# Performance work log

Measured on AMD Instinct MI355X. Metric: run time of the kernel, lower is better.

Reference implementation:

```python
import jax, jax.numpy as jnp
import numpy as np


def _lstm_layer(xs, W_ih, W_hh, b):
    # xs: [T, B, D]; W_ih: [4H, D]; W_hh: [4H, H]; b: [4H] (b_ih + b_hh)
    T, B, _ = xs.shape
    H = W_hh.shape[1]
    # precompute input projection for all timesteps: [T, B, 4H]
    x_proj = jnp.einsum('tbd,gd->tbg', xs, W_ih) + b

    def step(carry, xp):
        h, c = carry
        gates = xp + h @ W_hh.T                      # [B, 4H]
        i, f, g, o = jnp.split(gates, 4, axis=-1)    # torch gate order i,f,g,o
        i = jax.nn.sigmoid(i)
        f = jax.nn.sigmoid(f)
        g = jnp.tanh(g)
        o = jax.nn.sigmoid(o)
        c = f * c + i * g
        h = o * jnp.tanh(c)
        return (h, c), h

    h0 = jnp.zeros((B, H), xs.dtype)
    c0 = jnp.zeros((B, H), xs.dtype)
    (h_T, c_T), outs = jax.lax.scan(step, (h0, c0), x_proj)
    return outs, h_T, c_T  # outs: [T, B, H]


def setup_inputs() -> dict:
    key = jax.random.key(0)
    ks = jax.random.split(key, 8)
    B, T, D, H, C = 64, 256, 512, 1024, 1000
    s = 0.05
    return {
        'x': jax.random.normal(ks[0], (B, T, D), jnp.float32),
        'W_ih0': jax.random.normal(ks[1], (4 * H, D), jnp.float32) * s,
        'W_hh0': jax.random.normal(ks[2], (4 * H, H), jnp.float32) * s,
        'b_ih0': jnp.zeros((4 * H,), jnp.float32),
        'b_hh0': jnp.zeros((4 * H,), jnp.float32),
        'W_ih1': jax.random.normal(ks[3], (4 * H, H), jnp.float32) * s,
        'W_hh1': jax.random.normal(ks[4], (4 * H, H), jnp.float32) * s,
        'b_ih1': jnp.zeros((4 * H,), jnp.float32),
        'b_hh1': jnp.zeros((4 * H,), jnp.float32),
        'W_fc': jax.random.normal(ks[5], (C, 2 * H), jnp.float32) * s,
        'b_fc': jnp.zeros((C,), jnp.float32),
    }


def reference(x, W_ih0, W_hh0, b_ih0, b_hh0, W_ih1, W_hh1, b_ih1, b_hh1, W_fc, b_fc):
    # x: [B, T, D] -> time-major [T, B, D]
    xs = jnp.swapaxes(x, 0, 1)
    outs0, h0_T, _ = _lstm_layer(xs, W_ih0, W_hh0, b_ih0 + b_hh0)
    # inter-layer dropout is identity at inference
    outs1, h1_T, _ = _lstm_layer(outs0, W_ih1, W_hh1, b_ih1 + b_hh1)
    # concat final hidden states of all layers: [B, 2H]
    h_final = jnp.concatenate([h0_T, h1_T], axis=-1)
    logits = h_final @ W_fc.T + b_fc  # [B, C]
    return logits
```

## Files before the change

kernel.cpp:

```cpp
#include <hip/hip_runtime.h>

#define BB 64
#define TT 256
#define DD 512
#define HH 1024
#define NCLS 1000

#define NB   256
#define L0B  128
#define COLS 8
#define RING 64
#define HSZ  (BB * HH)
#define CHK0 48
#define CHK1 64
#define TS0  (CHK0 * 512)
#define TS1  (CHK1 * 512)
#define GRP  32
#define EPSLP 4
#define DYNLDS (2 * TS1 * 2 + 4 * 64 * 9 * 4 + 64 * 8 * 2)
#define BARWORDS ((2 * L0B + 2 * GRP) * 32)

typedef _Float16 f16;
typedef _Float16 f16x4 __attribute__((ext_vector_type(4)));
typedef _Float16 f16x8 __attribute__((ext_vector_type(8)));
typedef float f32x4 __attribute__((ext_vector_type(4)));
typedef int i32x4 __attribute__((ext_vector_type(4)));

#define MFMA16(af, bf, acc) __builtin_amdgcn_mfma_f32_16x16x32_f16((af), (bf), (acc), 0, 0, 0)
#define FSIG(x) (1.f / (1.f + __expf(-(x))))
#define FTANH(x) (1.f - 2.f / (__expf(2.f * (x)) + 1.f))
#define ALOAD __HIP_MEMORY_SCOPE_AGENT

template <int N, int I = 0>
__device__ __forceinline__ void glP(i32x4* A, const f16* base) {
  if constexpr (I < N) {
    asm volatile("global_load_dwordx4 %0, %1, off offset:%2"
                 : "=v"(A[I]) : "v"(base + (I >> 2) * 2048), "n"((I & 3) * 1024));
    glP<N, I + 1>(A, base);
  }
}
template <int TOTAL, int EXTRA, int BBASE, int G = 0>
__device__ __forceinline__ void mf2(i32x4* A, const f16* w0, const f16* w1,
                                    f32x4& a0, f32x4& a1, f32x4& b0, f32x4& b1) {
  if constexpr (G * 8 < TOTAL) {
    asm volatile("s_waitcnt vmcnt(%0)" :: "n"(TOTAL - (G + 1) * 8 + EXTRA)
                 : "memory");
    __builtin_amdgcn_sched_barrier(0);
    #pragma unroll
    for (int k = 0; k < 8; ++k) {
      int ck = G * 8 + k;
      f16x8 a;
      __builtin_memcpy(&a, &A[ck], 16);
      const f16* p0 = w0 + (size_t)(BBASE + ck) * 512;
      const f16* p1 = w1 + (size_t)(BBASE + ck) * 512;
      if (ck & 1) {
        a1 = MFMA16(a, *(const f16x8*)p0, a1);
        b1 = MFMA16(a, *(const f16x8*)p1, b1);
      } else {
        a0 = MFMA16(a, *(const f16x8*)p0, a0);
        b0 = MFMA16(a, *(const f16x8*)p1, b0);
      }
    }
    mf2<TOTAL, EXTRA, BBASE, G + 1>(A, w0, w1, a0, a1, b0, b1);
  }
}

__global__ __launch_bounds__(256) void prep_x_kernel(const float* __restrict__ x,
                                                     f16* __restrict__ xpk) {
  int idx = blockIdx.x * 256 + threadIdx.x;
  int seg = idx & 63;
  int b   = (idx >> 6) & 63;
  int t   = idx >> 12;
  float4 u = *(const float4*)(x + ((size_t)b * TT + t) * DD + seg * 8);
  float4 v = *(const float4*)(x + ((size_t)b * TT + t) * DD + seg * 8 + 4);
  f16x8 o = {(f16)u.x, (f16)u.y, (f16)u.z, (f16)u.w,
             (f16)v.x, (f16)v.y, (f16)v.z, (f16)v.w};
  int ch = seg >> 2, kgrp = seg & 3;
  *(f16x8*)(xpk + ((size_t)((t * 4 + (b >> 4)) * 16 + ch) * 64 +
                   kgrp * 16 + (b & 15)) * 8) = o;
}

__global__ __launch_bounds__(512, 2) void lstm_persistent(
    const f16* __restrict__ xpk,
    const float* __restrict__ Wih0, const float* __restrict__ Whh0,
    const float* __restrict__ bih0, const float* __restrict__ bhh0,
    const float* __restrict__ Wih1, const float* __restrict__ Whh1,
    const float* __restrict__ bih1, const float* __restrict__ bhh1,
    f16* __restrict__ h0ring, f16* __restrict__ h1ring, int* __restrict__ bar) {
  extern __shared__ f16 lds[];
  const int bid  = blockIdx.x;
  const bool IS1 = (bid >= L0B);
  const int j0   = (IS1 ? bid - L0B : bid) * COLS;
  const int tid  = threadIdx.x;
  const int wv   = tid >> 6;
  const int lane = tid & 63;
  const int kh   = wv >> 2;
  const int bt   = wv & 3;
  const int col  = lane & 15;
  const int kgrp = lane >> 4;
  const int jc   = col & 7;
  const int ch0  = j0 >> 5;
  const int kg0  = (j0 >> 3) & 3;

  const int CHK = IS1 ? CHK1 : CHK0;
  const int TS  = IS1 ? TS1 : TS0;
  const int DIN = IS1 ? HH : DD;
  f16* Wpk    = lds;
  float* pbuf = (float*)(lds + 2 * TS1);
  f16* hbuf   = (f16*)(pbuf + 4 * 64 * 9);

  {
    const float* Wi = IS1 ? Wih1 : Wih0;
    const float* Wh = IS1 ? Whh1 : Whh0;
    const int grow = (kh * 2 + (col >> 3)) * HH + j0 + jc;
    const float* rowi = Wi + (size_t)grow * DIN;
    const float* rowh = Wh + (size_t)grow * HH;
    for (int ck = bt; ck < CHK; ck += 4) {
      int k = ck * 32 + kgrp * 8;
      const float* src = (k < DIN) ? (rowi + k) : (rowh + (k - DIN));
      float4 u = *(const float4*)src;
      float4 v = *(const float4*)(src + 4);
      f16x8 w = {(f16)u.x, (f16)u.y, (f16)u.z, (f16)u.w,
                 (f16)v.x, (f16)v.y, (f16)v.z, (f16)v.w};
      *(f16x8*)(Wpk + (size_t)kh * TS + (size_t)ck * 512 + lane * 8) = w;
    }
  }
  const float* bi = IS1 ? bih1 : bih0;
  const float* bh = IS1 ? bhh1 : bhh0;
  const int g0 = (col < 8) ? 0 : 1;
  const int g1 = (col < 8) ? 2 : 3;
  const float bias0 = bi[g0 * HH + j0 + jc] + bh[g0 * HH + j0 + jc];
  const float bias1 = bi[g1 * HH + j0 + jc] + bh[g1 * HH + j0 + jc];
  __syncthreads();

  float creg[4] = {0.f, 0.f, 0.f, 0.f};
  int* flag0 = bar;
  int* flag1 = bar + L0B * 32;
  int* ep0   = bar + 2 * L0B * 32;
  int* ep1   = ep0 + GRP * 32;
  const int myrep = (IS1 ? bid - L0B : bid) & (GRP - 1);
  const f16* w0 = Wpk + lane * 8;
  const f16* w1 = Wpk + (size_t)TS + lane * 8;

  auto cellstore = [&](f32x4 aA0, f32x4 aA1, f32x4 aB0, f32x4 aB1, f16* hw) {
    if (kh == 1) {
      #pragma unroll
      for (int r = 0; r < 4; ++r) {
        pbuf[((size_t)bt * 64 + lane) * 9 + r]     = aA0[r] + aA1[r];
        pbuf[((size_t)bt * 64 + lane) * 9 + 4 + r] = aB0[r] + aB1[r];
      }
    }
    __syncthreads();
    if (kh == 0) {
      #pragma unroll
      for (int r = 0; r < 4; ++r) {
        float pv0 = aA0[r] + aA1[r] + pbuf[((size_t)bt * 64 + lane) * 9 + r] + bias0;
        float pv1 = aB0[r] + aB1[r] + pbuf[((size_t)bt * 64 + lane) * 9 + 4 + r] + bias1;
        float q0 = __shfl_xor(pv0, 8);
        float q1 = __shfl_xor(pv1, 8);
        if (col < 8) {
          float ig = FSIG(pv0);
          float fg = FSIG(q0);
          float gg = FTANH(pv1);
          float og = FSIG(q1);
          float cc = fg * creg[r] + ig * gg;
          creg[r] = cc;
          hbuf[((size_t)bt * 16 + kgrp * 4 + r) * 8 + jc] = (f16)(og * FTANH(cc));
        }
      }
      if (lane < 16) {
        f16x8 hv = *(const f16x8*)(hbuf + ((size_t)bt * 16 + lane) * 8);
        f16* dst = hw + ((size_t)(bt * 32 + ch0) * 64 + kg0 * 16 + lane) * 8;
        i32x4 hvi;
        __builtin_memcpy(&hvi, &hv, 16);
        asm volatile("global_store_dwordx4 %0, %1, off sc1"
                     :: "v"(dst), "v"(hvi) : "memory");
      }
    }
  };

  if (!IS1) {
    const bool AGG = (bid == 0);
    i32x4 afs[16];
    i32x4 afc[16];
    if (kh == 0)
      glP<16>(afs, xpk + (size_t)(0 * 4 + bt) * 16 * 512 + lane * 8);
    for (int t = 0; t < TT; ++t) {
      if (AGG) {
        if (tid < L0B)
          while (__hip_atomic_load(flag0 + tid * 32, __ATOMIC_RELAXED, ALOAD) < t)
            __builtin_amdgcn_s_sleep(1);
      } else if (tid == 0) {
        while (__hip_atomic_load(ep0 + myrep * 32, __ATOMIC_RELAXED, ALOAD) < t)
          __builtin_amdgcn_s_sleep(EPSLP);
      }
      if (tid == 256) {
        while (__hip_atomic_load(ep1 + myrep * 32, __ATOMIC_RELAXED, ALOAD) < t - (RING - 1))
          __builtin_amdgcn_s_sleep(EPSLP);
      }
      __syncthreads();
      if (AGG && tid < GRP)
        __hip_atomic_store(ep0 + tid * 32, t, __ATOMIC_RELAXED, ALOAD);
      const f16* hp = h0ring + (size_t)((t - 1) & (RING - 1)) * HSZ +
                      (size_t)(bt * 32 + kh * 16) * 512 + lane * 8;
      f32x4 aA0 = {0.f,0.f,0.f,0.f}, aA1 = {0.f,0.f,0.f,0.f};
      f32x4 aB0 = {0.f,0.f,0.f,0.f}, aB1 = {0.f,0.f,0.f,0.f};
      if (kh == 0) {
        glP<16>(afc, hp);
        mf2<16, 16, 0>(afs, w0, w1, aA0, aA1, aB0, aB1);
        mf2<16, 0, 16>(afc, w0, w1, aA0, aA1, aB0, aB1);
      } else {
        glP<16>(afc, hp);
        mf2<16, 0, 32>(afc, w0, w1, aA0, aA1, aB0, aB1);
      }
      cellstore(aA0, aA1, aB0, aB1, h0ring + (size_t)(t & (RING - 1)) * HSZ);
      asm volatile("s_waitcnt vmcnt(0)" ::: "memory");
      __syncthreads();
      if (tid == 0)
        __hip_atomic_store(flag0 + bid * 32, t + 1, __ATOMIC_RELAXED, ALOAD);
      if (kh == 0 && t + 1 < TT)
        glP<16>(afs, xpk + (size_t)((t + 1) * 4 + bt) * 16 * 512 + lane * 8);
    }
    if (AGG) {
      if (tid < L0B)
        while (__hip_atomic_load(flag0 + tid * 32, __ATOMIC_RELAXED, ALOAD) < TT)
          __builtin_amdgcn_s_sleep(1);
      __syncthreads();
      if (tid < GRP)
        __hip_atomic_store(ep0 + tid * 32, TT, __ATOMIC_RELAXED, ALOAD);
    }
  } else {
    const bool AGG = (bid == L0B);
    i32x4 afs[32];
    i32x4 afc[16];
    {
      if (tid == 0)
        while (__hip_atomic_load(ep0 + myrep * 32, __ATOMIC_RELAXED, ALOAD) < 1)
          __builtin_amdgcn_s_sleep(EPSLP);
      __syncthreads();
      if (kh == 0)
        glP<32>(afs, h0ring + (size_t)0 * HSZ + (size_t)bt * 32 * 512 + lane * 8);
    }
    for (int u = 0; u < TT; ++u) {
      if (AGG) {
        if (tid < L0B)
          while (__hip_atomic_load(flag1 + tid * 32, __ATOMIC_RELAXED, ALOAD) < u)
            __builtin_amdgcn_s_sleep(1);
        __syncthreads();
        if (tid < GRP)
          __hip_atomic_store(ep1 + tid * 32, u, __ATOMIC_RELAXED, ALOAD);
      } else {
        if (tid == 0)
          while (__hip_atomic_load(ep1 + myrep * 32, __ATOMIC_RELAXED, ALOAD) < u)
            __builtin_amdgcn_s_sleep(EPSLP);
        __syncthreads();
      }
      const f16* h1p = h1ring + (size_t)((u - 1) & (RING - 1)) * HSZ +
                       (size_t)(bt * 32 + kh * 16) * 512 + lane * 8;
      f32x4 aA0 = {0.f,0.f,0.f,0.f}, aA1 = {0.f,0.f,0.f,0.f};
      f32x4 aB0 = {0.f,0.f,0.f,0.f}, aB1 = {0.f,0.f,0.f,0.f};
      if (kh == 0) {
        glP<16>(afc, h1p);
        mf2<32, 16, 0>(afs, w0, w1, aA0, aA1, aB0, aB1);
        mf2<16, 0, 32>(afc, w0, w1, aA0, aA1, aB0, aB1);
      } else {
        glP<16>(afc, h1p);
        mf2<16, 0, 48>(afc, w0, w1, aA0, aA1, aB0, aB1);
      }
      cellstore(aA0, aA1, aB0, aB1, h1ring + (size_t)(u & (RING - 1)) * HSZ);
      asm volatile("s_waitcnt vmcnt(0)" ::: "memory");
      __syncthreads();
      if (tid == 0)
        __hip_atomic_store(flag1 + (bid - L0B) * 32, u + 1, __ATOMIC_RELAXED, ALOAD);
      if (u + 1 < TT) {
        if (tid == 256)
          while (__hip_atomic_load(ep0 + myrep * 32, __ATOMIC_RELAXED, ALOAD) < u + 2)
            __builtin_amdgcn_s_sleep(EPSLP);
        __syncthreads();
        if (kh == 0)
          glP<32>(afs, h0ring + (size_t)((u + 1) & (RING - 1)) * HSZ +
                       (size_t)bt * 32 * 512 + lane * 8);
      }
    }
  }
}

__global__ __launch_bounds__(256) void fc_kernel(const f16* __restrict__ h0f,
                                                 const f16* __restrict__ h1f,
                                                 const float* __restrict__ Wfc,
                                                 const float* __restrict__ bfc,
                                                 float* __restrict__ out) {
  __shared__ f16 hl[64][264];
  __shared__ float Wl[4][260];
  const int tid = threadIdx.x;
  const int cl0 = blockIdx.x * 4;
  const int b   = tid >> 2;
  const int cq  = tid & 3;
  float a = 0.f;
  for (int k0 = 0; k0 < 2 * HH; k0 += 256) {
    #pragma unroll
    for (int i = 0; i < 8; i++) {
      int v   = tid + i * 256;
      int row = v >> 5;
      int kk  = (v & 31) * 8;
      int kg  = k0 + kk;
      int kg2 = (kg < HH) ? kg : kg - HH;
      const f16* bse = (kg < HH) ? h0f : h1f;
      const f16* src = bse + ((size_t)((row >> 4) * 32 + (kg2 >> 5)) * 64 +
                              ((kg2 >> 3) & 3) * 16 + (row & 15)) * 8;
      *(f16x8*)(&hl[row][kk]) = *(const f16x8*)src;
    }
    {
      int row = tid >> 6;
      int kk  = (tid & 63) * 4;
      *(float4*)(&Wl[row][kk]) = *(const float4*)(Wfc + (size_t)(cl0 + row) * (2 * HH) + k0 + kk);
    }
    __syncthreads();
    #pragma unroll 8
    for (int k = 0; k < 256; k++) a += (float)hl[b][k] * Wl[cq][k];
    __syncthreads();
  }
  out[(size_t)b * NCLS + cl0 + cq] = a + bfc[cl0 + cq];
}

extern "C" void kernel_launch(void* const* d_in, const int* in_sizes, int n_in,
                              void* d_out, int out_size, void* d_ws, size_t ws_size,
                              hipStream_t stream) {
  const float* x    = (const float*)d_in[0];
  const float* Wih0 = (const float*)d_in[1];
  const float* Whh0 = (const float*)d_in[2];
  const float* bih0 = (const float*)d_in[3];
  const float* bhh0 = (const float*)d_in[4];
  const float* Wih1 = (const float*)d_in[5];
  const float* Whh1 = (const float*)d_in[6];
  const float* bih1 = (const float*)d_in[7];
  const float* bhh1 = (const float*)d_in[8];
  const float* Wfc  = (const float*)d_in[9];
  const float* bfc  = (const float*)d_in[10];
  float* out = (float*)d_out;

  char* p = (char*)d_ws;
  auto alloc = [&](size_t bytes) {
    char* r = p;
    p += (bytes + 255) & ~(size_t)255;
    return r;
  };
  f16* xpk    = (f16*)alloc((size_t)BB * TT * DD * 2);
  f16* h0ring = (f16*)alloc((size_t)RING * HSZ * 2);
  f16* h1ring = (f16*)alloc((size_t)RING * HSZ * 2);
  int* bar    = (int*)alloc((size_t)BARWORDS * 4);

  if ((size_t)(p - (char*)d_ws) > ws_size) return;

  (void)hipMemsetAsync(bar, 0, (size_t)BARWORDS * 4, stream);
  (void)hipMemsetAsync(h0ring + (size_t)(RING - 1) * HSZ, 0, (size_t)HSZ * 2, stream);
  (void)hipMemsetAsync(h1ring + (size_t)(RING - 1) * HSZ, 0, (size_t)HSZ * 2, stream);

  prep_x_kernel<<<dim3(TT * BB * (DD / 8) / 256), dim3(256), 0, stream>>>(x, xpk);

  (void)hipFuncSetAttribute((const void*)lstm_persistent,
                            hipFuncAttributeMaxDynamicSharedMemorySize, DYNLDS);
  lstm_persistent<<<dim3(NB), dim3(512), DYNLDS, stream>>>(
      xpk, Wih0, Whh0, bih0, bhh0, Wih1, Whh1, bih1, bhh1, h0ring, h1ring, bar);

  fc_kernel<<<dim3(NCLS / 4), dim3(256), 0, stream>>>(
      h0ring + (size_t)(RING - 1) * HSZ, h1ring + (size_t)(RING - 1) * HSZ,
      Wfc, bfc, out);
}
```

Before: 1.350 ms.

## Replace aggregator-based grid barrier with per-block scout wavefronts and LDS signals

Drops the two-level epoch barrier, where one aggregator block polled all flags and republished them to group epoch words. Now every block has scout wavefronts that poll all 128 per-block flags directly (one lane per flag) and signal the other waves through LDS words. The layer-1 ring back-pressure and layer-0 readiness checks move into scouts and are waited on only where they are needed, so the per-step __syncthreads around the poll goes away. The intent is to cut the barrier latency on each recurrent step. In exchange every block now polls global flags, which adds memory traffic, and correctness rests on LDS spin ordering.

```diff
diff --git a/kernel.cpp b/kernel.cpp
--- a/kernel.cpp
+++ b/kernel.cpp
@@ -15,10 +15,8 @@
 #define CHK1 64
 #define TS0  (CHK0 * 512)
 #define TS1  (CHK1 * 512)
-#define GRP  32
-#define EPSLP 4
-#define DYNLDS (2 * TS1 * 2 + 4 * 64 * 9 * 4 + 64 * 8 * 2)
-#define BARWORDS ((2 * L0B + 2 * GRP) * 32)
+#define DYNLDS (2 * TS1 * 2 + 4 * 64 * 9 * 4 + 64 * 8 * 2 + 32)
+#define BARWORDS (2 * L0B * 32)
 
 typedef _Float16 f16;
 typedef _Float16 f16x4 __attribute__((ext_vector_type(4)));
@@ -63,6 +61,10 @@
     }
     mf2<TOTAL, EXTRA, BBASE, G + 1>(A, w0, w1, a0, a1, b0, b1);
   }
+}
+
+__device__ __forceinline__ void spin_lds(volatile int* p, int tgt) {
+  while (*p < tgt) __builtin_amdgcn_s_sleep(1);
 }
 
 __global__ __launch_bounds__(256) void prep_x_kernel(const float* __restrict__ x,
@@ -108,6 +110,8 @@
   f16* Wpk    = lds;
   float* pbuf = (float*)(lds + 2 * TS1);
   f16* hbuf   = (f16*)(pbuf + 4 * 64 * 9);
+  volatile int* sigR = (volatile int*)(hbuf + 64 * 8);
+  volatile int* sigX = sigR + 2;
 
   {
     const float* Wi = IS1 ? Wih1 : Wih0;
@@ -125,6 +129,7 @@
       *(f16x8*)(Wpk + (size_t)kh * TS + (size_t)ck * 512 + lane * 8) = w;
     }
   }
+  if (tid < 4) sigR[tid] = 0;
   const float* bi = IS1 ? bih1 : bih0;
   const float* bh = IS1 ? bhh1 : bhh0;
   const int g0 = (col < 8) ? 0 : 1;
@@ -136,13 +141,17 @@
   float creg[4] = {0.f, 0.f, 0.f, 0.f};
   int* flag0 = bar;
   int* flag1 = bar + L0B * 32;
-  int* ep0   = bar + 2 * L0B * 32;
-  int* ep1   = ep0 + GRP * 32;
-  const int myrep = (IS1 ? bid - L0B : bid) & (GRP - 1);
   const f16* w0 = Wpk + lane * 8;
   const f16* w1 = Wpk + (size_t)TS + lane * 8;
 
-  auto cellstore = [&](f32x4 aA0, f32x4 aA1, f32x4 aB0, f32x4 aB1, f16* hw) {
+  auto scout_poll = [&](int* flags_, int tgt) {
+    while (__hip_atomic_load(flags_ + (kh * 64 + lane) * 32, __ATOMIC_RELAXED,
+                             ALOAD) < tgt)
+      __builtin_amdgcn_s_sleep(1);
+  };
+
+  auto cellstore = [&](f32x4 aA0, f32x4 aA1, f32x4 aB0, f32x4 aB1, f16* hw,
+                       int gate) {
     if (kh == 1) {
       #pragma unroll
       for (int r = 0; r < 4; ++r) {
@@ -168,6 +177,7 @@
           hbuf[((size_t)bt * 16 + kgrp * 4 + r) * 8 + jc] = (f16)(og * FTANH(cc));
         }
       }
+      if (gate) { spin_lds(&sigX[0], gate); spin_lds(&sigX[1], gate); }
       if (lane < 16) {
         f16x8 hv = *(const f16x8*)(hbuf + ((size_t)bt * 16 + lane) * 8);
         f16* dst = hw + ((size_t)(bt * 32 + ch0) * 64 + kg0 * 16 + lane) * 8;
@@ -180,27 +190,19 @@
   };
 
   if (!IS1) {
-    const bool AGG = (bid == 0);
     i32x4 afs[16];
     i32x4 afc[16];
     if (kh == 0)
       glP<16>(afs, xpk + (size_t)(0 * 4 + bt) * 16 * 512 + lane * 8);
     for (int t = 0; t < TT; ++t) {
-      if (AGG) {
-        if (tid < L0B)
-          while (__hip_atomic_load(flag0 + tid * 32, __ATOMIC_RELAXED, ALOAD) < t)
-            __builtin_amdgcn_s_sleep(1);
-      } else if (tid == 0) {
-        while (__hip_atomic_load(ep0 + myrep * 32, __ATOMIC_RELAXED, ALOAD) < t)
-          __builtin_amdgcn_s_sleep(EPSLP);
-      }
-      if (tid == 256) {
-        while (__hip_atomic_load(ep1 + myrep * 32, __ATOMIC_RELAXED, ALOAD) < t - (RING - 1))
-          __builtin_amdgcn_s_sleep(EPSLP);
-      }
-      __syncthreads();
-      if (AGG && tid < GRP)
-        __hip_atomic_store(ep0 + tid * 32, t, __ATOMIC_RELAXED, ALOAD);
+      if (bt == 0) {
+        scout_poll(flag0, t);
+        if (lane == 0) sigR[kh] = t + 1;
+      } else if (bt == 1) {
+        scout_poll(flag1, t - (RING - 1));
+        if (lane == 0) sigX[kh] = t + 1;
+      }
+      spin_lds(&sigR[kh], t + 1);
       const f16* hp = h0ring + (size_t)((t - 1) & (RING - 1)) * HSZ +
                       (size_t)(bt * 32 + kh * 16) * 512 + lane * 8;
       f32x4 aA0 = {0.f,0.f,0.f,0.f}, aA1 = {0.f,0.f,0.f,0.f};
@@ -213,7 +215,8 @@
         glP<16>(afc, hp);
         mf2<16, 0, 32>(afc, w0, w1, aA0, aA1, aB0, aB1);
       }
-      cellstore(aA0, aA1, aB0, aB1, h0ring + (size_t)(t & (RING - 1)) * HSZ);
+      cellstore(aA0, aA1, aB0, aB1, h0ring + (size_t)(t & (RING - 1)) * HSZ,
+                t + 1);
       asm volatile("s_waitcnt vmcnt(0)" ::: "memory");
       __syncthreads();
       if (tid == 0)
@@ -221,40 +224,29 @@
       if (kh == 0 && t + 1 < TT)
         glP<16>(afs, xpk + (size_t)((t + 1) * 4 + bt) * 16 * 512 + lane * 8);
     }
-    if (AGG) {
-      if (tid < L0B)
-        while (__hip_atomic_load(flag0 + tid * 32, __ATOMIC_RELAXED, ALOAD) < TT)
-          __builtin_amdgcn_s_sleep(1);
-      __syncthreads();
-      if (tid < GRP)
-        __hip_atomic_store(ep0 + tid * 32, TT, __ATOMIC_RELAXED, ALOAD);
-    }
   } else {
-    const bool AGG = (bid == L0B);
     i32x4 afs[32];
     i32x4 afc[16];
     {
-      if (tid == 0)
-        while (__hip_atomic_load(ep0 + myrep * 32, __ATOMIC_RELAXED, ALOAD) < 1)
-          __builtin_amdgcn_s_sleep(EPSLP);
-      __syncthreads();
-      if (kh == 0)
+      if (bt == 1) {
+        scout_poll(flag0, 1);
+        if (lane == 0) sigX[kh] = 1;
+      }
+      if (kh == 0) {
+        spin_lds(&sigX[0], 1);
+        spin_lds(&sigX[1], 1);
         glP<32>(afs, h0ring + (size_t)0 * HSZ + (size_t)bt * 32 * 512 + lane * 8);
+      }
     }
     for (int u = 0; u < TT; ++u) {
-      if (AGG) {
-        if (tid < L0B)
-          while (__hip_atomic_load(flag1 + tid * 32, __ATOMIC_RELAXED, ALOAD) < u)
-            __builtin_amdgcn_s_sleep(1);
-        __syncthreads();
-        if (tid < GRP)
-          __hip_atomic_store(ep1 + tid * 32, u, __ATOMIC_RELAXED, ALOAD);
-      } else {
-        if (tid == 0)
-          while (__hip_atomic_load(ep1 + myrep * 32, __ATOMIC_RELAXED, ALOAD) < u)
-            __builtin_amdgcn_s_sleep(EPSLP);
-        __syncthreads();
-      }
+      if (bt == 0) {
+        scout_poll(flag1, u);
+        if (lane == 0) sigR[kh] = u + 1;
+      } else if (bt == 1 && u + 1 < TT) {
+        scout_poll(flag0, u + 2);
+        if (lane == 0) sigX[kh] = u + 2;
+      }
+      spin_lds(&sigR[kh], u + 1);
       const f16* h1p = h1ring + (size_t)((u - 1) & (RING - 1)) * HSZ +
                        (size_t)(bt * 32 + kh * 16) * 512 + lane * 8;
       f32x4 aA0 = {0.f,0.f,0.f,0.f}, aA1 = {0.f,0.f,0.f,0.f};
@@ -267,19 +259,16 @@
         glP<16>(afc, h1p);
         mf2<16, 0, 48>(afc, w0, w1, aA0, aA1, aB0, aB1);
       }
-      cellstore(aA0, aA1, aB0, aB1, h1ring + (size_t)(u & (RING - 1)) * HSZ);
+      cellstore(aA0, aA1, aB0, aB1, h1ring + (size_t)(u & (RING - 1)) * HSZ, 0);
       asm volatile("s_waitcnt vmcnt(0)" ::: "memory");
       __syncthreads();
       if (tid == 0)
         __hip_atomic_store(flag1 + (bid - L0B) * 32, u + 1, __ATOMIC_RELAXED, ALOAD);
-      if (u + 1 < TT) {
-        if (tid == 256)
-          while (__hip_atomic_load(ep0 + myrep * 32, __ATOMIC_RELAXED, ALOAD) < u + 2)
-            __builtin_amdgcn_s_sleep(EPSLP);
-        __syncthreads();
-        if (kh == 0)
-          glP<32>(afs, h0ring + (size_t)((u + 1) & (RING - 1)) * HSZ +
-                       (size_t)bt * 32 * 512 + lane * 8);
+      if (kh == 0 && u + 1 < TT) {
+        spin_lds(&sigX[0], u + 2);
+        spin_lds(&sigX[1], u + 2);
+        glP<32>(afs, h0ring + (size_t)((u + 1) & (RING - 1)) * HSZ +
+                     (size_t)bt * 32 * 512 + lane * 8);
       }
     }
   }
```

New measurement: 1.460 ms. 8.1% more time.

## Split input-projection MFMA across both K-halves and issue it before the recurrence wait

Applied to the files above, without the earlier changes.

The input-side contribution (x projection for layer 0, layer-0 output for layer 1) is now divided evenly between the two kh halves instead of done entirely by kh==0. It is also computed at the top of each timestep, before the spin-wait on the previous step's h. The aim is to balance MFMA work between waves and take the input-side GEMM off the serial recurrence critical path. Register use for the prefetched fragments is halved per wave. The risk is that accumulating before the wait changes register pressure and the issue schedule.

```diff
diff --git a/kernel.cpp b/kernel.cpp
--- a/kernel.cpp
+++ b/kernel.cpp
@@ -181,11 +181,15 @@
 
   if (!IS1) {
     const bool AGG = (bid == 0);
-    i32x4 afs[16];
+    i32x4 afs[8];
     i32x4 afc[16];
-    if (kh == 0)
-      glP<16>(afs, xpk + (size_t)(0 * 4 + bt) * 16 * 512 + lane * 8);
+    glP<8>(afs, xpk + (size_t)(0 * 4 + bt) * 16 * 512 +
+                (size_t)kh * 8 * 512 + lane * 8);
     for (int t = 0; t < TT; ++t) {
+      f32x4 aA0 = {0.f,0.f,0.f,0.f}, aA1 = {0.f,0.f,0.f,0.f};
+      f32x4 aB0 = {0.f,0.f,0.f,0.f}, aB1 = {0.f,0.f,0.f,0.f};
+      if (kh == 0) mf2<8, 0, 0>(afs, w0, w1, aA0, aA1, aB0, aB1);
+      else         mf2<8, 0, 8>(afs, w0, w1, aA0, aA1, aB0, aB1);
       if (AGG) {
         if (tid < L0B)
           while (__hip_atomic_load(flag0 + tid * 32, __ATOMIC_RELAXED, ALOAD) < t)
@@ -203,23 +207,17 @@
         __hip_atomic_store(ep0 + tid * 32, t, __ATOMIC_RELAXED, ALOAD);
       const f16* hp = h0ring + (size_t)((t - 1) & (RING - 1)) * HSZ +
                       (size_t)(bt * 32 + kh * 16) * 512 + lane * 8;
-      f32x4 aA0 = {0.f,0.f,0.f,0.f}, aA1 = {0.f,0.f,0.f,0.f};
-      f32x4 aB0 = {0.f,0.f,0.f,0.f}, aB1 = {0.f,0.f,0.f,0.f};
-      if (kh == 0) {
-        glP<16>(afc, hp);
-        mf2<16, 16, 0>(afs, w0, w1, aA0, aA1, aB0, aB1);
-        mf2<16, 0, 16>(afc, w0, w1, aA0, aA1, aB0, aB1);
-      } else {
-        glP<16>(afc, hp);
-        mf2<16, 0, 32>(afc, w0, w1, aA0, aA1, aB0, aB1);
-      }
+      glP<16>(afc, hp);
+      if (kh == 0) mf2<16, 0, 16>(afc, w0, w1, aA0, aA1, aB0, aB1);
+      else         mf2<16, 0, 32>(afc, w0, w1, aA0, aA1, aB0, aB1);
       cellstore(aA0, aA1, aB0, aB1, h0ring + (size_t)(t & (RING - 1)) * HSZ);
       asm volatile("s_waitcnt vmcnt(0)" ::: "memory");
       __syncthreads();
       if (tid == 0)
         __hip_atomic_store(flag0 + bid * 32, t + 1, __ATOMIC_RELAXED, ALOAD);
-      if (kh == 0 && t + 1 < TT)
-        glP<16>(afs, xpk + (size_t)((t + 1) * 4 + bt) * 16 * 512 + lane * 8);
+      if (t + 1 < TT)
+        glP<8>(afs, xpk + (size_t)((t + 1) * 4 + bt) * 16 * 512 +
+                    (size_t)kh * 8 * 512 + lane * 8);
     }
     if (AGG) {
       if (tid < L0B)
@@ -231,17 +229,21 @@
     }
   } else {
     const bool AGG = (bid == L0B);
-    i32x4 afs[32];
+    i32x4 afs[16];
     i32x4 afc[16];
     {
       if (tid == 0)
         while (__hip_atomic_load(ep0 + myrep * 32, __ATOMIC_RELAXED, ALOAD) < 1)
           __builtin_amdgcn_s_sleep(EPSLP);
       __syncthreads();
-      if (kh == 0)
-        glP<32>(afs, h0ring + (size_t)0 * HSZ + (size_t)bt * 32 * 512 + lane * 8);
+      glP<16>(afs, h0ring + (size_t)0 * HSZ +
+                   (size_t)(bt * 32 + kh * 16) * 512 + lane * 8);
     }
     for (int u = 0; u < TT; ++u) {
+      f32x4 aA0 = {0.f,0.f,0.f,0.f}, aA1 = {0.f,0.f,0.f,0.f};
+      f32x4 aB0 = {0.f,0.f,0.f,0.f}, aB1 = {0.f,0.f,0.f,0.f};
+      if (kh == 0) mf2<16, 0, 0>(afs, w0, w1, aA0, aA1, aB0, aB1);
+      else         mf2<16, 0, 16>(afs, w0, w1, aA0, aA1, aB0, aB1);
       if (AGG) {
         if (tid < L0B)
           while (__hip_atomic_load(flag1 + tid * 32, __ATOMIC_RELAXED, ALOAD) < u)
@@ -257,16 +259,9 @@
       }
       const f16* h1p = h1ring + (size_t)((u - 1) & (RING - 1)) * HSZ +
                        (size_t)(bt * 32 + kh * 16) * 512 + lane * 8;
-      f32x4 aA0 = {0.f,0.f,0.f,0.f}, aA1 = {0.f,0.f,0.f,0.f};
-      f32x4 aB0 = {0.f,0.f,0.f,0.f}, aB1 = {0.f,0.f,0.f,0.f};
-      if (kh == 0) {
-        glP<16>(afc, h1p);
-        mf2<32, 16, 0>(afs, w0, w1, aA0, aA1, aB0, aB1);
-        mf2<16, 0, 32>(afc, w0, w1, aA0, aA1, aB0, aB1);
-      } else {
-        glP<16>(afc, h1p);
-        mf2<16, 0, 48>(afc, w0, w1, aA0, aA1, aB0, aB1);
-      }
+      glP<16>(afc, h1p);
+      if (kh == 0) mf2<16, 0, 32>(afc, w0, w1, aA0, aA1, aB0, aB1);
+      else         mf2<16, 0, 48>(afc, w0, w1, aA0, aA1, aB0, aB1);
       cellstore(aA0, aA1, aB0, aB1, h1ring + (size_t)(u & (RING - 1)) * HSZ);
       asm volatile("s_waitcnt vmcnt(0)" ::: "memory");
       __syncthreads();
@@ -277,9 +272,8 @@
           while (__hip_atomic_load(ep0 + myrep * 32, __ATOMIC_RELAXED, ALOAD) < u + 2)
             __builtin_amdgcn_s_sleep(EPSLP);
         __syncthreads();
-        if (kh == 0)
-          glP<32>(afs, h0ring + (size_t)((u + 1) & (RING - 1)) * HSZ +
-                       (size_t)bt * 32 * 512 + lane * 8);
+        glP<16>(afs, h0ring + (size_t)((u + 1) & (RING - 1)) * HSZ +
+                     (size_t)(bt * 32 + kh * 16) * 512 + lane * 8);
       }
     }
   }
```

After: 1.391 ms. +3.1%, slower.
